# Kernel tuning notes

Hardware: AMD Instinct MI355X
Metric: run time of the kernel (lower is better)

Reference implementation:

```python
import jax, jax.numpy as jnp
import numpy as np

E = 100000
VERTEX_DIM = 64
EDGE_DIM = 128
MESSAGE_DIM = 64


def setup_inputs() -> dict:
    key = jax.random.key(0)
    k1, k2, k3, k4 = jax.random.split(key, 4)
    vertices = jax.random.normal(k1, (E, VERTEX_DIM), dtype=jnp.float32)
    edges = jax.random.normal(k2, (E, EDGE_DIM), dtype=jnp.float32)
    # nn.Linear(edge_dim, message_dim * vertex_dim): weight [out, in], bias [out]
    W = jax.random.normal(k3, (MESSAGE_DIM * VERTEX_DIM, EDGE_DIM), dtype=jnp.float32) * (1.0 / np.sqrt(EDGE_DIM))
    b = jax.random.normal(k4, (MESSAGE_DIM * VERTEX_DIM,), dtype=jnp.float32) * 0.01
    return {"vertices": vertices, "edges": edges, "W": W, "b": b}


def reference(vertices, edges, W, b):
    # edge_net(edges): [E, message_dim*vertex_dim]
    proj = edges @ W.T + b
    # view to [E, message_dim, vertex_dim], then batched matvec with vertices [E, vertex_dim]
    proj = proj.reshape(edges.shape[0], MESSAGE_DIM, VERTEX_DIM)
    message = jnp.einsum('emv,ev->em', proj, vertices)  # [E, message_dim]
    return message
```

## Files before the change

### kernel.cpp

```cpp
#include <hip/hip_runtime.h>
#include <stdint.h>


typedef _Float16 f16;
typedef __attribute__((ext_vector_type(2))) _Float16 f16x2;
typedef __attribute__((ext_vector_type(8))) _Float16 f16x8;
typedef __attribute__((ext_vector_type(4))) float f32x4;

#define MSG_D 64
#define VTX_D 64
#define EDG_D 128

__device__ __forceinline__ f16x8 cvt8(float4 a, float4 d) {
  return (f16x8){(f16)a.x, (f16)a.y, (f16)a.z, (f16)a.w,
                 (f16)d.x, (f16)d.y, (f16)d.z, (f16)d.w};
}

__global__ void prep_w(const float* __restrict__ W, const float* __restrict__ b,
                       f16* __restrict__ Wh, f16* __restrict__ Bh) {
  int tid = blockIdx.x * 256 + threadIdx.x;
  if (tid < 65536) {
    int L = tid & 63, n = (tid >> 6) & 3, s = (tid >> 8) & 3, v = tid >> 10;
    int q = L >> 4, ln = L & 15;
    const float* src = W + (size_t)((n * 16 + ln) * 64 + v) * 128 + s * 32 + q * 8;
    float4 a = *(const float4*)src, d = *(const float4*)(src + 4);
    *(f16x8*)(Wh + (size_t)tid * 8) = cvt8(a, d);
  } else if (tid < 66048) {
    int t2 = tid - 65536;
    int L = t2 & 63, n = (t2 >> 6) & 3, s2 = t2 >> 8;
    int q = L >> 4, ln = L & 15;
    const float* src = b + (n * 16 + ln) * 64 + s2 * 32 + q * 8;
    float4 a = *(const float4*)src, d = *(const float4*)(src + 4);
    *(f16x8*)(Bh + (size_t)t2 * 8) = cvt8(a, d);
  }
}

typedef __attribute__((address_space(1))) const void GV;
typedef __attribute__((address_space(3))) void LV;
__device__ __forceinline__ void gload_lds16(const void* g, void* l) {
  __builtin_amdgcn_global_load_lds((GV*)g, (LV*)l, 16, 0, 0);
}

__global__ __launch_bounds__(256, 2) void edge_msg_lds(
    const float* __restrict__ Vtx, const float* __restrict__ Xe,
    const f16* __restrict__ Wh, const f16* __restrict__ Bh,
    float* __restrict__ out, int E)
{
  __shared__ f16 Wsh[3 * 8192];
  __shared__ f16 Vt[64 * 256];

  const int tid = threadIdx.x;
  const int wid = tid >> 6, lane = tid & 63;
  const int q = lane >> 4, ln = lane & 15;
  const int eblk = blockIdx.x * 256;
  const int eoff = eblk + wid * 64;

  int er[4];
  f16x8 xh[4][4];
  #pragma unroll
  for (int t = 0; t < 4; ++t) {
    int e = eoff + 16 * t + ln;
    er[t] = e < E ? e : E - 1;
    const float* xr = Xe + (size_t)er[t] * EDG_D;
    #pragma unroll
    for (int s = 0; s < 4; ++s) {
      float4 a = *(const float4*)(xr + s * 32 + q * 8);
      float4 d = *(const float4*)(xr + s * 32 + q * 8 + 4);
      xh[t][s] = cvt8(a, d);
    }
  }

  {
    int e = eblk + tid;
    int ec = e < E ? e : E - 1;
    const float* vr = Vtx + (size_t)ec * VTX_D;
    #pragma unroll
    for (int k = 0; k < 16; ++k) {
      float4 a = *(const float4*)(vr + k * 4);
      Vt[(k * 4 + 0) * 256 + tid] = (f16)a.x;
      Vt[(k * 4 + 1) * 256 + tid] = (f16)a.y;
      Vt[(k * 4 + 2) * 256 + tid] = (f16)a.z;
      Vt[(k * 4 + 3) * 256 + tid] = (f16)a.w;
    }
  }

  f32x4 acc[4][4];
  #pragma unroll
  for (int t = 0; t < 4; ++t)
    #pragma unroll
    for (int n = 0; n < 4; ++n) acc[t][n] = (f32x4){0.f, 0.f, 0.f, 0.f};

  asm volatile("s_waitcnt lgkmcnt(0)" ::: "memory");
  __builtin_amdgcn_s_barrier();
  asm volatile("" ::: "memory");

  {
    const char* gbase = (const char*)Wh + (size_t)(wid * 4) * 1024 + (size_t)lane * 16;
    char* lbase = (char*)&Wsh[0] + (wid * 4) * 1024;
    #pragma unroll
    for (int c = 0; c < 4; ++c) gload_lds16(gbase + c * 1024, lbase + c * 1024);
    #pragma unroll
    for (int c = 0; c < 4; ++c)
      gload_lds16(gbase + 16384 + c * 1024, lbase + 2 * 8192 + c * 1024);
  }

  int bo = 0;

  #pragma unroll 1
  for (int v = 0; v < 64; ++v) {
    if (v == 63) asm volatile("s_waitcnt vmcnt(0)" ::: "memory");
    else         asm volatile("s_waitcnt vmcnt(4)" ::: "memory");
    __builtin_amdgcn_s_barrier();
    asm volatile("" ::: "memory");

    if (v < 62) {
      int so = bo + 2 * 8192;
      if (so >= 3 * 8192) so -= 3 * 8192;
      const char* gbase = (const char*)Wh + (size_t)(v + 2) * 16384 +
                          (size_t)(wid * 4) * 1024 + (size_t)lane * 16;
      char* lbase = (char*)&Wsh[so] + (wid * 4) * 1024;
      #pragma unroll
      for (int c = 0; c < 4; ++c) gload_lds16(gbase + c * 1024, lbase + c * 1024);
    }

    f16x2 hv[4];
    #pragma unroll
    for (int t = 0; t < 4; ++t) {
      f16 h = Vt[v * 256 + wid * 64 + 16 * t + ln];
      hv[t] = (f16x2){h, h};
    }

    const f16* wb = &Wsh[bo + lane * 8];
    #pragma unroll
    for (int s = 0; s < 4; ++s) {
      f16x8 bf[4];
      #pragma unroll
      for (int n = 0; n < 4; ++n) bf[n] = *(const f16x8*)(wb + (s * 4 + n) * 512);

      f16x8 af[4];
      #pragma unroll
      for (int t = 0; t < 4; ++t) {
        union { f16x8 v8; f16x2 h2[4]; } x, r;
        x.v8 = xh[t][s];
        r.h2[0] = hv[t] * x.h2[0];
        r.h2[1] = hv[t] * x.h2[1];
        r.h2[2] = hv[t] * x.h2[2];
        r.h2[3] = hv[t] * x.h2[3];
        af[t] = r.v8;
      }
      #pragma unroll
      for (int n = 0; n < 4; ++n)
        #pragma unroll
        for (int t = 0; t < 4; ++t)
          acc[t][n] = __builtin_amdgcn_mfma_f32_16x16x32_f16(af[t], bf[n], acc[t][n], 0, 0, 0);
    }

    bo += 8192;
    if (bo >= 3 * 8192) bo -= 3 * 8192;
  }

  #pragma unroll
  for (int s2 = 0; s2 < 2; ++s2) {
    f16x8 av[4];
    #pragma unroll
    for (int t = 0; t < 4; ++t) {
      const float* vr2 = Vtx + (size_t)er[t] * VTX_D + s2 * 32 + q * 8;
      float4 a = *(const float4*)vr2, d = *(const float4*)(vr2 + 4);
      av[t] = cvt8(a, d);
    }
    #pragma unroll
    for (int n = 0; n < 4; ++n) {
      f16x8 bfb = *(const f16x8*)(Bh + (size_t)((s2 * 4 + n) * 64 + lane) * 8);
      #pragma unroll
      for (int t = 0; t < 4; ++t)
        acc[t][n] = __builtin_amdgcn_mfma_f32_16x16x32_f16(av[t], bfb, acc[t][n], 0, 0, 0);
    }
  }

  #pragma unroll
  for (int t = 0; t < 4; ++t)
    #pragma unroll
    for (int r = 0; r < 4; ++r) {
      int e = eoff + 16 * t + 4 * q + r;
      if (e < E) {
        float* orow = out + (size_t)e * MSG_D;
        #pragma unroll
        for (int n = 0; n < 4; ++n) orow[n * 16 + ln] = acc[t][n][r];
      }
    }
}

__global__ void edge_msg_naive(const float* __restrict__ Vtx, const float* __restrict__ Xe,
                               const float* __restrict__ W, const float* __restrict__ b,
                               float* __restrict__ out, int E) {
  __shared__ float xs[EDG_D];
  __shared__ float vs[VTX_D];
  int e = blockIdx.x;
  int m = threadIdx.x;
  for (int i = m; i < EDG_D; i += 64) xs[i] = Xe[(size_t)e * EDG_D + i];
  for (int i = m; i < VTX_D; i += 64) vs[i] = Vtx[(size_t)e * VTX_D + i];
  __syncthreads();
  float s = 0.f;
  for (int v = 0; v < VTX_D; ++v) {
    const float* wr = W + (size_t)(m * 64 + v) * EDG_D;
    float p = b[m * 64 + v];
    for (int k = 0; k < EDG_D; ++k) p += xs[k] * wr[k];
    s += p * vs[v];
  }
  out[(size_t)e * MSG_D + m] = s;
}

extern "C" void kernel_launch(void* const* d_in, const int* in_sizes, int n_in,
                              void* d_out, int out_size, void* d_ws, size_t ws_size,
                              hipStream_t stream) {
  const float* Vtx = (const float*)d_in[0];
  const float* Xe  = (const float*)d_in[1];
  const float* W   = (const float*)d_in[2];
  const float* b   = (const float*)d_in[3];
  float* out = (float*)d_out;

  const int E  = in_sizes[0] / VTX_D;
  const int nW = in_sizes[2];
  const int nb = in_sizes[3];

  const size_t needW = (size_t)(524288 + 4096) * sizeof(f16);

  if (nW != 524288 || nb != 4096 || ws_size < needW) {
    edge_msg_naive<<<E, 64, 0, stream>>>(Vtx, Xe, W, b, out, E);
    return;
  }

  f16* Wh = (f16*)d_ws;
  f16* Bh = Wh + 524288;

  prep_w<<<258, 256, 0, stream>>>(W, b, Wh, Bh);

  int blocks = (E + 255) / 256;
  edge_msg_lds<<<blocks, 256, 0, stream>>>(Vtx, Xe, Wh, Bh, out, E);
}
```

Before: 206.0 us.

## Split output columns across wave pairs, halve edge tile, finer W ring for occupancy

Each block now handles 128 edges with two waves per 64-edge group, each covering half of the message columns, which halves the accumulator registers and LDS per block and allows three blocks per CU. The W pipeline streams half-v chunks through a four-slot ring with a three-deep prefetch, and the MFMA section is wrapped in setprio. The cost is that each wave reloads and rescales the same edge features per v-step, so redundant A-fragment work doubles relative to MFMA work, and there are twice as many barriers per block.

```diff
diff --git a/kernel.cpp b/kernel.cpp
--- a/kernel.cpp
+++ b/kernel.cpp
@@ -41,19 +41,20 @@
   __builtin_amdgcn_global_load_lds((GV*)g, (LV*)l, 16, 0, 0);
 }
 
-__global__ __launch_bounds__(256, 2) void edge_msg_lds(
+__global__ __launch_bounds__(256, 3) void edge_msg_lds(
     const float* __restrict__ Vtx, const float* __restrict__ Xe,
     const f16* __restrict__ Wh, const f16* __restrict__ Bh,
     float* __restrict__ out, int E)
 {
-  __shared__ f16 Wsh[3 * 8192];
-  __shared__ f16 Vt[64 * 256];
+  __shared__ f16 Wring[4 * 4096];
+  __shared__ f16 Vt[64 * 128];
 
   const int tid = threadIdx.x;
   const int wid = tid >> 6, lane = tid & 63;
   const int q = lane >> 4, ln = lane & 15;
-  const int eblk = blockIdx.x * 256;
-  const int eoff = eblk + wid * 64;
+  const int h = wid >> 1, nh = wid & 1;
+  const int eblk = blockIdx.x * 128;
+  const int eoff = eblk + h * 64;
 
   int er[4];
   f16x8 xh[4][4];
@@ -71,72 +72,86 @@
   }
 
   {
-    int e = eblk + tid;
-    int ec = e < E ? e : E - 1;
-    const float* vr = Vtx + (size_t)ec * VTX_D;
-    #pragma unroll
-    for (int k = 0; k < 16; ++k) {
-      float4 a = *(const float4*)(vr + k * 4);
-      Vt[(k * 4 + 0) * 256 + tid] = (f16)a.x;
-      Vt[(k * 4 + 1) * 256 + tid] = (f16)a.y;
-      Vt[(k * 4 + 2) * 256 + tid] = (f16)a.z;
-      Vt[(k * 4 + 3) * 256 + tid] = (f16)a.w;
-    }
-  }
-
-  f32x4 acc[4][4];
+    int el = tid & 127;
+    int e2 = eblk + el;
+    int ec = e2 < E ? e2 : E - 1;
+    int vbase = (tid >> 7) * 32;
+    const float* vr = Vtx + (size_t)ec * VTX_D + vbase;
+    #pragma unroll
+    for (int k8 = 0; k8 < 4; ++k8) {
+      float4 a = *(const float4*)(vr + k8 * 8);
+      float4 d = *(const float4*)(vr + k8 * 8 + 4);
+      int v = vbase + k8 * 8;
+      Vt[(v + 0) * 128 + el] = (f16)a.x;
+      Vt[(v + 1) * 128 + el] = (f16)a.y;
+      Vt[(v + 2) * 128 + el] = (f16)a.z;
+      Vt[(v + 3) * 128 + el] = (f16)a.w;
+      Vt[(v + 4) * 128 + el] = (f16)d.x;
+      Vt[(v + 5) * 128 + el] = (f16)d.y;
+      Vt[(v + 6) * 128 + el] = (f16)d.z;
+      Vt[(v + 7) * 128 + el] = (f16)d.w;
+    }
+  }
+
+  f32x4 acc[4][2];
   #pragma unroll
   for (int t = 0; t < 4; ++t)
     #pragma unroll
-    for (int n = 0; n < 4; ++n) acc[t][n] = (f32x4){0.f, 0.f, 0.f, 0.f};
+    for (int nn = 0; nn < 2; ++nn) acc[t][nn] = (f32x4){0.f, 0.f, 0.f, 0.f};
+
+  {
+    const size_t wl = (size_t)(wid * 2) * 1024 + (size_t)lane * 16;
+    #pragma unroll
+    for (int k = 0; k < 3; ++k) {
+      const char* g = (const char*)Wh + (size_t)(k >> 1) * 16384 + (size_t)(k & 1) * 8192 + wl;
+      char* l = (char*)&Wring[(k & 3) * 4096] + (wid * 2) * 1024;
+      gload_lds16(g, l);
+      gload_lds16(g + 1024, l + 1024);
+    }
+  }
 
   asm volatile("s_waitcnt lgkmcnt(0)" ::: "memory");
   __builtin_amdgcn_s_barrier();
   asm volatile("" ::: "memory");
 
-  {
-    const char* gbase = (const char*)Wh + (size_t)(wid * 4) * 1024 + (size_t)lane * 16;
-    char* lbase = (char*)&Wsh[0] + (wid * 4) * 1024;
-    #pragma unroll
-    for (int c = 0; c < 4; ++c) gload_lds16(gbase + c * 1024, lbase + c * 1024);
-    #pragma unroll
-    for (int c = 0; c < 4; ++c)
-      gload_lds16(gbase + 16384 + c * 1024, lbase + 2 * 8192 + c * 1024);
-  }
-
-  int bo = 0;
-
   #pragma unroll 1
-  for (int v = 0; v < 64; ++v) {
-    if (v == 63) asm volatile("s_waitcnt vmcnt(0)" ::: "memory");
-    else         asm volatile("s_waitcnt vmcnt(4)" ::: "memory");
+  for (int k = 0; k < 128; ++k) {
+    const int v = k >> 1, p = k & 1;
+
+    if (k == 127)      asm volatile("s_waitcnt vmcnt(0)" ::: "memory");
+    else if (k == 126) asm volatile("s_waitcnt vmcnt(2)" ::: "memory");
+    else               asm volatile("s_waitcnt vmcnt(4)" ::: "memory");
     __builtin_amdgcn_s_barrier();
     asm volatile("" ::: "memory");
 
-    if (v < 62) {
-      int so = bo + 2 * 8192;
-      if (so >= 3 * 8192) so -= 3 * 8192;
-      const char* gbase = (const char*)Wh + (size_t)(v + 2) * 16384 +
-                          (size_t)(wid * 4) * 1024 + (size_t)lane * 16;
-      char* lbase = (char*)&Wsh[so] + (wid * 4) * 1024;
-      #pragma unroll
-      for (int c = 0; c < 4; ++c) gload_lds16(gbase + c * 1024, lbase + c * 1024);
+    if (k < 125) {
+      const int k3 = k + 3;
+      const char* g = (const char*)Wh + (size_t)(k3 >> 1) * 16384 + (size_t)(k3 & 1) * 8192 +
+                      (size_t)(wid * 2) * 1024 + (size_t)lane * 16;
+      char* l = (char*)&Wring[(k3 & 3) * 4096] + (wid * 2) * 1024;
+      gload_lds16(g, l);
+      gload_lds16(g + 1024, l + 1024);
     }
 
     f16x2 hv[4];
     #pragma unroll
     for (int t = 0; t < 4; ++t) {
-      f16 h = Vt[v * 256 + wid * 64 + 16 * t + ln];
-      hv[t] = (f16x2){h, h};
-    }
-
-    const f16* wb = &Wsh[bo + lane * 8];
-    #pragma unroll
-    for (int s = 0; s < 4; ++s) {
-      f16x8 bf[4];
-      #pragma unroll
-      for (int n = 0; n < 4; ++n) bf[n] = *(const f16x8*)(wb + (s * 4 + n) * 512);
-
+      f16 hh = Vt[v * 128 + h * 64 + 16 * t + ln];
+      hv[t] = (f16x2){hh, hh};
+    }
+
+    __builtin_amdgcn_s_setprio(1);
+    const f16* wb = &Wring[(k & 3) * 4096 + lane * 8];
+    f16x8 bf[4];
+    #pragma unroll
+    for (int sl = 0; sl < 2; ++sl)
+      #pragma unroll
+      for (int nn = 0; nn < 2; ++nn)
+        bf[sl * 2 + nn] = *(const f16x8*)(wb + (sl * 4 + 2 * nh + nn) * 512);
+
+    #pragma unroll
+    for (int sl = 0; sl < 2; ++sl) {
+      const int s = 2 * p + sl;
       f16x8 af[4];
       #pragma unroll
       for (int t = 0; t < 4; ++t) {
@@ -149,14 +164,12 @@
         af[t] = r.v8;
       }
       #pragma unroll
-      for (int n = 0; n < 4; ++n)
+      for (int nn = 0; nn < 2; ++nn)
         #pragma unroll
         for (int t = 0; t < 4; ++t)
-          acc[t][n] = __builtin_amdgcn_mfma_f32_16x16x32_f16(af[t], bf[n], acc[t][n], 0, 0, 0);
-    }
-
-    bo += 8192;
-    if (bo >= 3 * 8192) bo -= 3 * 8192;
+          acc[t][nn] = __builtin_amdgcn_mfma_f32_16x16x32_f16(af[t], bf[sl * 2 + nn], acc[t][nn], 0, 0, 0);
+    }
+    __builtin_amdgcn_s_setprio(0);
   }
 
   #pragma unroll
@@ -169,11 +182,12 @@
       av[t] = cvt8(a, d);
     }
     #pragma unroll
-    for (int n = 0; n < 4; ++n) {
+    for (int nn = 0; nn < 2; ++nn) {
+      const int n = 2 * nh + nn;
       f16x8 bfb = *(const f16x8*)(Bh + (size_t)((s2 * 4 + n) * 64 + lane) * 8);
       #pragma unroll
       for (int t = 0; t < 4; ++t)
-        acc[t][n] = __builtin_amdgcn_mfma_f32_16x16x32_f16(av[t], bfb, acc[t][n], 0, 0, 0);
+        acc[t][nn] = __builtin_amdgcn_mfma_f32_16x16x32_f16(av[t], bfb, acc[t][nn], 0, 0, 0);
     }
   }
 
@@ -185,7 +199,7 @@
       if (e < E) {
         float* orow = out + (size_t)e * MSG_D;
         #pragma unroll
-        for (int n = 0; n < 4; ++n) orow[n * 16 + ln] = acc[t][n][r];
+        for (int nn = 0; nn < 2; ++nn) orow[(2 * nh + nn) * 16 + ln] = acc[t][nn][r];
       }
     }
 }
@@ -235,6 +249,6 @@
 
   prep_w<<<258, 256, 0, stream>>>(W, b, Wh, Bh);
 
-  int blocks = (E + 255) / 256;
+  int blocks = (E + 127) / 128;
   edge_msg_lds<<<blocks, 256, 0, stream>>>(Vtx, Xe, Wh, Bh, out, E);
 }
```

Measured after the change: 646.6 us. 214% more time.
